# Kernel optimization log

Measured on AMD Instinct MI355X. Metric: run time of the kernel, lower is better.

Reference implementation:

```python
import jax, jax.numpy as jnp
import numpy as np

B, T, D_IN, H, D_OUT, L = 256, 512, 64, 512, 1, 2


def _lstm_layer(xs, W_ih, W_hh, b):
    """xs: [T, B, D]; W_ih: [4H, D]; W_hh: [4H, H]; b: [4H] (b_ih + b_hh).
    PyTorch gate order: i, f, g, o. Returns (ys [T,B,H], h_T [B,H])."""
    Bsz = xs.shape[1]
    Hh = W_hh.shape[1]
    h0 = jnp.zeros((Bsz, Hh), xs.dtype)
    c0 = jnp.zeros((Bsz, Hh), xs.dtype)

    def step(carry, x_t):
        h, c = carry
        gates = x_t @ W_ih.T + h @ W_hh.T + b  # [B, 4H]
        i, f, g, o = jnp.split(gates, 4, axis=-1)
        i = jax.nn.sigmoid(i)
        f = jax.nn.sigmoid(f)
        g = jnp.tanh(g)
        o = jax.nn.sigmoid(o)
        c = f * c + i * g
        h = o * jnp.tanh(c)
        return (h, c), h

    (hT, _), ys = jax.lax.scan(step, (h0, c0), xs)
    return ys, hT


def setup_inputs() -> dict:
    key = jax.random.key(0)
    ks = jax.random.split(key, 12)
    s = 0.05  # small init to avoid gate saturation
    return {
        "x": jax.random.normal(ks[0], (B, T, D_IN), jnp.float32),
        "W_ih0": jax.random.normal(ks[1], (4 * H, D_IN), jnp.float32) * s,
        "W_hh0": jax.random.normal(ks[2], (4 * H, H), jnp.float32) * s,
        "b0": jax.random.normal(ks[3], (4 * H,), jnp.float32) * s,
        "W_ih1": jax.random.normal(ks[4], (4 * H, H), jnp.float32) * s,
        "W_hh1": jax.random.normal(ks[5], (4 * H, H), jnp.float32) * s,
        "b1": jax.random.normal(ks[6], (4 * H,), jnp.float32) * s,
        "fc1_w": jax.random.normal(ks[7], (H, H), jnp.float32) * s,
        "fc1_b": jax.random.normal(ks[8], (H,), jnp.float32) * s,
        "fc_w": jax.random.normal(ks[9], (D_OUT, H), jnp.float32) * s,
        "fc_b": jax.random.normal(ks[10], (D_OUT,), jnp.float32) * s,
    }


def reference(x, W_ih0, W_hh0, b0, W_ih1, W_hh1, b1, fc1_w, fc1_b, fc_w, fc_b):
    xs = jnp.swapaxes(x, 0, 1)  # [T, B, D_IN]
    ys0, _ = _lstm_layer(xs, W_ih0, W_hh0, b0)      # [T, B, H]
    _, hT = _lstm_layer(ys0, W_ih1, W_hh1, b1)      # [B, H] == out[:, -1, :]
    h = jax.nn.relu(hT @ fc1_w.T + fc1_b)
    out = jax.nn.relu(h @ fc_w.T + fc_b)
    return out
```

## Files before the change

kernel.cpp:

```cpp
#include <hip/hip_runtime.h>
#include <stdint.h>


typedef __bf16 bf16;
typedef bf16  bf16x8 __attribute__((ext_vector_type(8)));
typedef float f32x4  __attribute__((ext_vector_type(4)));
typedef unsigned int u32;
typedef unsigned long long u64;

#define NB   256
#define NT   512
#define NDIN 64
#define NH   512
#define POLL_GUARD (1 << 20)
#define SLOT_BYTES ((size_t)NB * NH * 2)

static constexpr size_t OFF_XB   = 0;
static constexpr size_t OFF_WB0  = OFF_XB  + (size_t)NB*NT*NDIN*2;
static constexpr size_t OFF_WI0  = OFF_WB0 + (size_t)2048*512*2;
static constexpr size_t OFF_WI1  = OFF_WI0 + (size_t)2048*64*2;
static constexpr size_t OFF_WHS1 = OFF_WI1 + (size_t)2048*512*2;
static constexpr size_t OFF_Y0R  = OFF_WHS1+ (size_t)16*128*512*2;
static constexpr size_t OFF_R1   = OFF_Y0R + 2*SLOT_BYTES;
static constexpr size_t OFF_HT   = OFF_R1  + 2*SLOT_BYTES;
static constexpr size_t OFF_FLG  = OFF_HT  + (size_t)NB*NH*4;
static constexpr size_t WS_NEED  = OFF_FLG + 4096;

#define MFMA16(a,b,c) __builtin_amdgcn_mfma_f32_16x16x32_bf16(a,b,c,0,0,0)

__device__ __forceinline__ float fsigm(float x) {
    return __builtin_amdgcn_rcpf(1.0f + __builtin_amdgcn_exp2f(x * -1.442695041f));
}
__device__ __forceinline__ float ftanh(float x) {
    return 1.0f - 2.0f * __builtin_amdgcn_rcpf(1.0f + __builtin_amdgcn_exp2f(x * 2.885390082f));
}
__device__ __forceinline__ u32 pack_bf16(float a, float b) {
    union { bf16 h[2]; u32 u; } un;
    un.h[0] = (bf16)a; un.h[1] = (bf16)b;
    return un.u;
}
__device__ __forceinline__ bf16x8 asf(int4 x) {
    union { int4 i; bf16x8 v; } u; u.i = x; return u.v;
}

__device__ __forceinline__ void ld4_issue(const void* p0, const void* p1,
                                          const void* p2, const void* p3,
                                          int4& a, int4& b, int4& c, int4& d) {
    asm volatile(
        "global_load_dwordx4 %0, %4, off sc0 sc1\n\t"
        "global_load_dwordx4 %1, %5, off sc0 sc1\n\t"
        "global_load_dwordx4 %2, %6, off sc0 sc1\n\t"
        "global_load_dwordx4 %3, %7, off sc0 sc1"
        : "=&v"(a), "=&v"(b), "=&v"(c), "=&v"(d)
        : "v"(p0), "v"(p1), "v"(p2), "v"(p3)
        : "memory");
}
__device__ __forceinline__ void st64_cohr(void* p, u64 v) {
    asm volatile("global_store_dwordx2 %0, %1, off sc0 sc1" :: "v"(p), "v"(v) : "memory");
}
__device__ __forceinline__ void vm_drain() {
    asm volatile("s_waitcnt vmcnt(0)" ::: "memory");
    __builtin_amdgcn_sched_barrier(0);
}
__device__ __forceinline__ void ld_fence() {
    asm volatile("" ::: "memory");
    __builtin_amdgcn_sched_barrier(0);
}
__device__ __forceinline__ void poll64(const u32* f, u32 target) {
    int guard = 0;
    while (__hip_atomic_load(f, __ATOMIC_RELAXED, __HIP_MEMORY_SCOPE_AGENT) < target)
        if (++guard > POLL_GUARD) break;
}
__device__ __forceinline__ void ast32(u32* p, u32 v) {
    __hip_atomic_store(p, v, __ATOMIC_RELAXED, __HIP_MEMORY_SCOPE_AGENT);
}

__device__ __forceinline__ int wslot(int lr) {
    return ((lr >> 5) & 3) | (((lr >> 1) & 3) << 2);
}

__global__ void xcvt_kernel(const float* __restrict__ x, char* __restrict__ ws) {
    size_t i = ((size_t)blockIdx.x * 256 + threadIdx.x) * 8;
    float4 a = *(const float4*)(x + i);
    float4 b = *(const float4*)(x + i + 4);
    u32 p0 = pack_bf16(a.x, a.y), p1 = pack_bf16(a.z, a.w);
    u32 p2 = pack_bf16(b.x, b.y), p3 = pack_bf16(b.z, b.w);
    *(int4*)(ws + OFF_XB + i * 2) = make_int4((int)p0, (int)p1, (int)p2, (int)p3);
}

__global__ void prep_kernel(const float* __restrict__ Wih0f, const float* __restrict__ Whh0f,
                            const float* __restrict__ Wih1f, const float* __restrict__ Whh1f,
                            char* __restrict__ ws) {
    int idx = blockIdx.x * 256 + threadIdx.x;
    ((bf16*)(ws + OFF_WB0))[idx] = (bf16)Whh0f[idx];
    ((bf16*)(ws + OFF_WI1))[idx] = (bf16)Wih1f[idx];
    if (idx < 2048 * 64) ((bf16*)(ws + OFF_WI0))[idx] = (bf16)Wih0f[idx];
    int slice = idx >> 16;
    int lr    = (idx >> 9) & 127;
    int k     = idx & 511;
    int grow  = (lr >> 5) * 512 + slice * 32 + (lr & 31);
    ((bf16*)(ws + OFF_WHS1))[(size_t)slice * 65536 + lr * 512 + (k ^ (wslot(lr) << 3))] =
        (bf16)Whh1f[(size_t)grow * 512 + k];
}

__global__ __attribute__((amdgpu_waves_per_eu(1, 1))) __launch_bounds__(256)
void lstm_fused(const float* __restrict__ b0, const float* __restrict__ b1,
                char* __restrict__ ws) {
    extern __shared__ char smem[];
    char* WhLds = smem;
    char* hbufY = smem + 131072;
    char* hbufH = smem + 147456;

    const int tid = threadIdx.x;
    const int v = tid >> 6, l = tid & 63;
    const int l15 = l & 15, lhi = l >> 4, g = l & 3, csel = l15 >> 2;
    const int group = blockIdx.x >> 4, htile = blockIdx.x & 15;
    const int b0r = group * 16, hs = htile * 32;

    const bf16* xb = (const bf16*)(ws + OFF_XB);
    char* y0r = ws + OFF_Y0R;
    char* r1  = ws + OFF_R1;
    float* hT = (float*)(ws + OFF_HT);
    u32* FL = (u32*)(ws + OFF_FLG);
    const u32* myLine = FL + (size_t)group * 64;
    u32* peerF        = FL + (size_t)group * 64 + htile * 4 + v;

    {
        const char* wsrc = ws + OFF_WHS1 + (size_t)htile * 131072;
#pragma unroll
        for (int i = 0; i < 32; ++i) {
            int off = (tid + i * 256) * 16;
            *(int4*)(WhLds + off) = *(const int4*)(wsrc + off);
        }
    }

    const int wrow0 = g * 512 + hs + 8 * v + 2 * csel;
    const int wrow1 = wrow0 + 1;

    const bf16* wb0p = (const bf16*)(ws + OFF_WB0);
    const bf16* wi0p = (const bf16*)(ws + OFF_WI0);
    const bf16* wi1p = (const bf16*)(ws + OFF_WI1);
    int4 wb0[16][2], wib1[16][2];
#pragma unroll
    for (int kk = 0; kk < 16; ++kk) {
        wb0[kk][0]  = *(const int4*)(wb0p + (size_t)wrow0 * NH + kk * 32 + lhi * 8);
        wb0[kk][1]  = *(const int4*)(wb0p + (size_t)wrow1 * NH + kk * 32 + lhi * 8);
        wib1[kk][0] = *(const int4*)(wi1p + (size_t)wrow0 * NH + kk * 32 + lhi * 8);
        wib1[kk][1] = *(const int4*)(wi1p + (size_t)wrow1 * NH + kk * 32 + lhi * 8);
    }
    int4 wib0[2][2];
#pragma unroll
    for (int kk = 0; kk < 2; ++kk) {
        wib0[kk][0] = *(const int4*)(wi0p + (size_t)wrow0 * NDIN + kk * 32 + lhi * 8);
        wib0[kk][1] = *(const int4*)(wi0p + (size_t)wrow1 * NDIN + kk * 32 + lhi * 8);
    }
    const float b00 = b0[wrow0], b01 = b0[wrow1];
    const float b10 = b1[wrow0], b11 = b1[wrow1];

    float cA0[4] = {0,0,0,0}, cA1[4] = {0,0,0,0};
    float cB0[4] = {0,0,0,0}, cB1[4] = {0,0,0,0};
    f32x4 aL00, aL01, aL10, aL11;
    const int qb = l & 60;
    const int srcl = csel * 16 + g;
    const int swz = (l15 & 7) << 4;
    const int lr0 = g * 32 + 8 * v + 2 * csel;
    const int wsw = wslot(lr0) << 4;
    const int r0 = tid >> 6;
    const int bc = (tid & 63) * 16;

    int4 G0, G1, G2, G3;
    int4 H0, H1, H2, H3;

    auto issueG = [&](int slot) {
        const char* p = y0r + (size_t)slot * SLOT_BYTES + (size_t)b0r * 1024
                      + (size_t)r0 * 1024 + bc;
        ld4_issue(p, p + 4096, p + 8192, p + 12288, G0, G1, G2, G3);
    };
    auto issueH = [&](int slot) {
        const char* p = r1 + (size_t)slot * SLOT_BYTES + (size_t)b0r * 1024
                      + (size_t)r0 * 1024 + bc;
        ld4_issue(p, p + 4096, p + 8192, p + 12288, H0, H1, H2, H3);
    };
    auto ldsWrite = [&](char* buf, int4 A, int4 B, int4 C, int4 D) {
        *(int4*)(buf + (r0     ) * 1024 + (bc ^ (( r0      & 7) << 4))) = A;
        *(int4*)(buf + (r0 +  4) * 1024 + (bc ^ (((r0 + 4) & 7) << 4))) = B;
        *(int4*)(buf + (r0 +  8) * 1024 + (bc ^ (( r0      & 7) << 4))) = C;
        *(int4*)(buf + (r0 + 12) * 1024 + (bc ^ (((r0 + 4) & 7) << 4))) = D;
    };
    auto xproj0 = [&](int t) {
        const bf16* xp = xb + ((size_t)(b0r + l15) * NT + t) * NDIN + lhi * 8;
        bf16x8 xa0 = *(const bf16x8*)xp;
        bf16x8 xa1 = *(const bf16x8*)(xp + 32);
        aL00 = f32x4{b00, b00, b00, b00};
        aL01 = f32x4{b01, b01, b01, b01};
        aL00 = MFMA16(xa0, asf(wib0[0][0]), aL00); aL00 = MFMA16(xa1, asf(wib0[1][0]), aL00);
        aL01 = MFMA16(xa0, asf(wib0[0][1]), aL01); aL01 = MFMA16(xa1, asf(wib0[1][1]), aL01);
    };
    auto combine = [&](const f32x4& a0, const f32x4& a1, float* cc0, float* cc1,
                       float& h0s, float& h1s) {
        h0s = 0.f; h1s = 0.f;
#pragma unroll
        for (int j = 0; j < 4; ++j) {
            float va = a0[j];
            float gi = __shfl(va, qb), gf = __shfl(va, qb + 1);
            float gc = __shfl(va, qb + 2), go = __shfl(va, qb + 3);
            float cn = fsigm(gf) * cc0[j] + fsigm(gi) * ftanh(gc);
            cc0[j] = cn;
            float h = fsigm(go) * ftanh(cn);
            if (j == g) h0s = h;
            float vb = a1[j];
            gi = __shfl(vb, qb); gf = __shfl(vb, qb + 1);
            gc = __shfl(vb, qb + 2); go = __shfl(vb, qb + 3);
            cn = fsigm(gf) * cc1[j] + fsigm(gi) * ftanh(gc);
            cc1[j] = cn;
            h = fsigm(go) * ftanh(cn);
            if (j == g) h1s = h;
        }
    };
    auto publish = [&](float h0s, float h1s, char* tileBase) {
        u32 pk = pack_bf16(h0s, h1s);
        u32 w0 = __shfl(pk, srcl),     w1 = __shfl(pk, srcl + 4);
        u32 w2 = __shfl(pk, srcl + 8), w3 = __shfl(pk, srcl + 12);
        if (l < 16) {
            char* rp = tileBase + (size_t)l * 1024 + hs * 2 + v * 16;
            union { u32 w[2]; u64 q; } qa, qb2;
            qa.w[0] = w0; qa.w[1] = w1; qb2.w[0] = w2; qb2.w[1] = w3;
            st64_cohr(rp, qa.q); st64_cohr(rp + 8, qb2.q);
        }
    };
    auto setF = [&](u32 val) {
        if (l == 0) ast32(peerF, val);
    };

    __syncthreads();

    xproj0(0);
    {
        float h0s, h1s;
        combine(aL00, aL01, cA0, cA1, h0s, h1s);
        publish(h0s, h1s, y0r + (size_t)b0r * 1024);
        vm_drain();
        setF(1u);
        xproj0(1);
    }

    for (int e = 1; e <= NT; ++e) {
        const bool doL0 = (e < NT);
        const bool doH1 = (e >= 2);

        poll64(myLine + l, (u32)e);
        ld_fence();
        issueG((e - 1) & 1);
        if (doH1) issueH(e & 1);
        vm_drain();

        __syncthreads();
        ldsWrite(hbufY, G0, G1, G2, G3);
        if (doH1) ldsWrite(hbufH, H0, H1, H2, H3);
        __syncthreads();

        aL10 = f32x4{b10, b10, b10, b10};
        aL11 = f32x4{b11, b11, b11, b11};
#pragma unroll
        for (int kk = 0; kk < 16; ++kk) {
            bf16x8 ha = *(const bf16x8*)(hbufY + l15 * 1024 + ((kk * 64 + lhi * 16) ^ swz));
            if (doL0) {
                aL00 = MFMA16(ha, asf(wb0[kk][0]), aL00);
                aL01 = MFMA16(ha, asf(wb0[kk][1]), aL01);
            }
            aL10 = MFMA16(ha, asf(wib1[kk][0]), aL10);
            aL11 = MFMA16(ha, asf(wib1[kk][1]), aL11);
        }

        if (doL0) {
            float h0s, h1s;
            combine(aL00, aL01, cA0, cA1, h0s, h1s);
            publish(h0s, h1s, y0r + (size_t)(e & 1) * SLOT_BYTES + (size_t)b0r * 1024);
        }

        if (doH1) {
#pragma unroll
            for (int kk = 0; kk < 16; ++kk) {
                int kb = kk * 64 + lhi * 16;
                bf16x8 a  = *(const bf16x8*)(hbufH + l15 * 1024 + (kb ^ swz));
                bf16x8 w0 = *(const bf16x8*)(WhLds + (size_t) lr0      * 1024 + (kb ^ wsw));
                bf16x8 w1 = *(const bf16x8*)(WhLds + (size_t)(lr0 + 1) * 1024 + (kb ^ wsw));
                aL10 = MFMA16(a, w0, aL10);
                aL11 = MFMA16(a, w1, aL11);
            }
        }

        {
            float h0s, h1s;
            combine(aL10, aL11, cB0, cB1, h0s, h1s);
            if (e < NT) {
                publish(h0s, h1s, r1 + (size_t)((e - 1) & 1) * SLOT_BYTES + (size_t)b0r * 1024);
            } else {
                float* hp = hT + (size_t)(b0r + lhi * 4 + g) * NH + hs + 8 * v + 2 * csel;
                hp[0] = h0s; hp[1] = h1s;
            }
        }
        if (e < NT) {
            vm_drain();
            setF((u32)(e + 1));
            xproj0(e + 1);
        }
    }
}

__global__ __launch_bounds__(256) void fc_kernel(const float* __restrict__ fc1_w,
                                                 const float* __restrict__ fc1_b,
                                                 const float* __restrict__ fc_w,
                                                 const float* __restrict__ fc_b,
                                                 const char* __restrict__ ws,
                                                 float* __restrict__ out) {
    __shared__ float hLds[512];
    __shared__ float red[256];
    const int b = blockIdx.x, tid = threadIdx.x;
    const float* hT = (const float*)(ws + OFF_HT) + (size_t)b * NH;
    hLds[tid]       = hT[tid];
    hLds[tid + 256] = hT[tid + 256];
    __syncthreads();
    float p = 0.f;
#pragma unroll
    for (int rep = 0; rep < 2; ++rep) {
        int hh = tid + rep * 256;
        const float* wr = fc1_w + (size_t)hh * 512;
        float s = fc1_b[hh];
        for (int k = 0; k < 512; k += 4) {
            float4 w4 = *(const float4*)(wr + k);
            s += hLds[k] * w4.x + hLds[k + 1] * w4.y + hLds[k + 2] * w4.z + hLds[k + 3] * w4.w;
        }
        s = fmaxf(s, 0.f);
        p += s * fc_w[hh];
    }
    red[tid] = p;
    __syncthreads();
    for (int off = 128; off > 0; off >>= 1) {
        if (tid < off) red[tid] += red[tid + off];
        __syncthreads();
    }
    if (tid == 0) out[b] = fmaxf(red[0] + fc_b[0], 0.f);
}

extern "C" void kernel_launch(void* const* d_in, const int* in_sizes, int n_in,
                              void* d_out, int out_size, void* d_ws, size_t ws_size,
                              hipStream_t stream) {
    const float* x    = (const float*)d_in[0];
    const float* Wih0 = (const float*)d_in[1];
    const float* Whh0 = (const float*)d_in[2];
    const float* b0   = (const float*)d_in[3];
    const float* Wih1 = (const float*)d_in[4];
    const float* Whh1 = (const float*)d_in[5];
    const float* b1   = (const float*)d_in[6];
    const float* fc1w = (const float*)d_in[7];
    const float* fc1b = (const float*)d_in[8];
    const float* fcw  = (const float*)d_in[9];
    const float* fcb  = (const float*)d_in[10];
    char* ws = (char*)d_ws;
    float* out = (float*)d_out;

    if (ws_size < WS_NEED) {
        (void)hipMemsetAsync(d_out, 0, (size_t)out_size * 4, stream);
        return;
    }

    (void)hipMemsetAsync(ws + OFF_FLG, 0, 4096, stream);

    hipLaunchKernelGGL(xcvt_kernel, dim3(4096), dim3(256), 0, stream, x, ws);
    hipLaunchKernelGGL(prep_kernel, dim3(4096), dim3(256), 0, stream,
                       Wih0, Whh0, Wih1, Whh1, ws);
    hipLaunchKernelGGL(lstm_fused, dim3(256), dim3(256), 163840, stream, b0, b1, ws);
    hipLaunchKernelGGL(fc_kernel, dim3(256), dim3(256), 0, stream,
                       fc1w, fc1b, fcw, fcb, ws, out);
}
```

Baseline: 3.071 ms.

## Split layer-0 and layer-1 LSTM work into separate warp groups with LDS flags

Doubles the block to 512 threads so four waves run layer 0 and four waves run layer 1 concurrently, each with its own global flag lines. Block-wide __syncthreads is replaced by LDS counter handshakes, and the layer-1 recurrent h buffer is staged in two halves to fit shared memory. The goal is to overlap the two layers' recurrences and cut per-step register pressure by giving each wave half the weights. The cost is two waves per SIMD, more complex spin-wait synchronisation, and some risk of ordering bugs.

```diff
diff --git a/kernel.cpp b/kernel.cpp
--- a/kernel.cpp
+++ b/kernel.cpp
@@ -24,7 +24,7 @@
 static constexpr size_t OFF_R1   = OFF_Y0R + 2*SLOT_BYTES;
 static constexpr size_t OFF_HT   = OFF_R1  + 2*SLOT_BYTES;
 static constexpr size_t OFF_FLG  = OFF_HT  + (size_t)NB*NH*4;
-static constexpr size_t WS_NEED  = OFF_FLG + 4096;
+static constexpr size_t WS_NEED  = OFF_FLG + 8192;
 
 #define MFMA16(a,b,c) __builtin_amdgcn_mfma_f32_16x16x32_bf16(a,b,c,0,0,0)
 
@@ -73,6 +73,14 @@
 }
 __device__ __forceinline__ void ast32(u32* p, u32 v) {
     __hip_atomic_store(p, v, __ATOMIC_RELAXED, __HIP_MEMORY_SCOPE_AGENT);
+}
+__device__ __forceinline__ void lds_pollge(const u32* p, u32 target) {
+    int guard = 0;
+    while (__hip_atomic_load(p, __ATOMIC_ACQUIRE, __HIP_MEMORY_SCOPE_WORKGROUP) < target)
+        if (++guard > POLL_GUARD) break;
+}
+__device__ __forceinline__ void lds_add1(u32* p) {
+    __hip_atomic_fetch_add(p, 1u, __ATOMIC_RELEASE, __HIP_MEMORY_SCOPE_WORKGROUP);
 }
 
 __device__ __forceinline__ int wslot(int lr) {
@@ -103,99 +111,55 @@
         (bf16)Whh1f[(size_t)grow * 512 + k];
 }
 
-__global__ __attribute__((amdgpu_waves_per_eu(1, 1))) __launch_bounds__(256)
+__global__ __attribute__((amdgpu_waves_per_eu(2, 2))) __launch_bounds__(512)
 void lstm_fused(const float* __restrict__ b0, const float* __restrict__ b1,
                 char* __restrict__ ws) {
     extern __shared__ char smem[];
     char* WhLds = smem;
-    char* hbufY = smem + 131072;
-    char* hbufH = smem + 147456;
+    char* ybuf  = smem + 131072;
+    char* hbuf8 = smem + 147456;
+    u32* ydone = (u32*)(smem + 155648);
+    u32* yrd   = ydone + 16;
+    u32* hdone = ydone + 32;
+    u32* hrd   = ydone + 48;
 
     const int tid = threadIdx.x;
-    const int v = tid >> 6, l = tid & 63;
+    const int l = tid & 63;
+    const int v = (tid >> 6) & 3;
+    const bool isL0 = tid < 256;
     const int l15 = l & 15, lhi = l >> 4, g = l & 3, csel = l15 >> 2;
     const int group = blockIdx.x >> 4, htile = blockIdx.x & 15;
     const int b0r = group * 16, hs = htile * 32;
+    const int qb = l & 60;
+    const int srcl = csel * 16 + g;
+    const int swz = (l15 & 7) << 4;
+    const int r0 = v;
+    const int bc = l * 16;
 
     const bf16* xb = (const bf16*)(ws + OFF_XB);
     char* y0r = ws + OFF_Y0R;
     char* r1  = ws + OFF_R1;
     float* hT = (float*)(ws + OFF_HT);
     u32* FL = (u32*)(ws + OFF_FLG);
-    const u32* myLine = FL + (size_t)group * 64;
-    u32* peerF        = FL + (size_t)group * 64 + htile * 4 + v;
-
+    const u32* lineY = FL + (size_t)group * 64;
+    const u32* lineH = FL + 1024 + (size_t)group * 64;
+    u32* peerFY = FL + (size_t)group * 64 + htile * 4 + v;
+    u32* peerFH = FL + 1024 + (size_t)group * 64 + htile * 4 + v;
+
+    if (tid == 0) { ydone[0] = 0; yrd[0] = 0; hdone[0] = 0; hrd[0] = 0; }
     {
         const char* wsrc = ws + OFF_WHS1 + (size_t)htile * 131072;
 #pragma unroll
-        for (int i = 0; i < 32; ++i) {
-            int off = (tid + i * 256) * 16;
+        for (int i = 0; i < 16; ++i) {
+            int off = (tid + i * 512) * 16;
             *(int4*)(WhLds + off) = *(const int4*)(wsrc + off);
         }
     }
+    __syncthreads();
 
     const int wrow0 = g * 512 + hs + 8 * v + 2 * csel;
     const int wrow1 = wrow0 + 1;
 
-    const bf16* wb0p = (const bf16*)(ws + OFF_WB0);
-    const bf16* wi0p = (const bf16*)(ws + OFF_WI0);
-    const bf16* wi1p = (const bf16*)(ws + OFF_WI1);
-    int4 wb0[16][2], wib1[16][2];
-#pragma unroll
-    for (int kk = 0; kk < 16; ++kk) {
-        wb0[kk][0]  = *(const int4*)(wb0p + (size_t)wrow0 * NH + kk * 32 + lhi * 8);
-        wb0[kk][1]  = *(const int4*)(wb0p + (size_t)wrow1 * NH + kk * 32 + lhi * 8);
-        wib1[kk][0] = *(const int4*)(wi1p + (size_t)wrow0 * NH + kk * 32 + lhi * 8);
-        wib1[kk][1] = *(const int4*)(wi1p + (size_t)wrow1 * NH + kk * 32 + lhi * 8);
-    }
-    int4 wib0[2][2];
-#pragma unroll
-    for (int kk = 0; kk < 2; ++kk) {
-        wib0[kk][0] = *(const int4*)(wi0p + (size_t)wrow0 * NDIN + kk * 32 + lhi * 8);
-        wib0[kk][1] = *(const int4*)(wi0p + (size_t)wrow1 * NDIN + kk * 32 + lhi * 8);
-    }
-    const float b00 = b0[wrow0], b01 = b0[wrow1];
-    const float b10 = b1[wrow0], b11 = b1[wrow1];
-
-    float cA0[4] = {0,0,0,0}, cA1[4] = {0,0,0,0};
-    float cB0[4] = {0,0,0,0}, cB1[4] = {0,0,0,0};
-    f32x4 aL00, aL01, aL10, aL11;
-    const int qb = l & 60;
-    const int srcl = csel * 16 + g;
-    const int swz = (l15 & 7) << 4;
-    const int lr0 = g * 32 + 8 * v + 2 * csel;
-    const int wsw = wslot(lr0) << 4;
-    const int r0 = tid >> 6;
-    const int bc = (tid & 63) * 16;
-
-    int4 G0, G1, G2, G3;
-    int4 H0, H1, H2, H3;
-
-    auto issueG = [&](int slot) {
-        const char* p = y0r + (size_t)slot * SLOT_BYTES + (size_t)b0r * 1024
-                      + (size_t)r0 * 1024 + bc;
-        ld4_issue(p, p + 4096, p + 8192, p + 12288, G0, G1, G2, G3);
-    };
-    auto issueH = [&](int slot) {
-        const char* p = r1 + (size_t)slot * SLOT_BYTES + (size_t)b0r * 1024
-                      + (size_t)r0 * 1024 + bc;
-        ld4_issue(p, p + 4096, p + 8192, p + 12288, H0, H1, H2, H3);
-    };
-    auto ldsWrite = [&](char* buf, int4 A, int4 B, int4 C, int4 D) {
-        *(int4*)(buf + (r0     ) * 1024 + (bc ^ (( r0      & 7) << 4))) = A;
-        *(int4*)(buf + (r0 +  4) * 1024 + (bc ^ (((r0 + 4) & 7) << 4))) = B;
-        *(int4*)(buf + (r0 +  8) * 1024 + (bc ^ (( r0      & 7) << 4))) = C;
-        *(int4*)(buf + (r0 + 12) * 1024 + (bc ^ (((r0 + 4) & 7) << 4))) = D;
-    };
-    auto xproj0 = [&](int t) {
-        const bf16* xp = xb + ((size_t)(b0r + l15) * NT + t) * NDIN + lhi * 8;
-        bf16x8 xa0 = *(const bf16x8*)xp;
-        bf16x8 xa1 = *(const bf16x8*)(xp + 32);
-        aL00 = f32x4{b00, b00, b00, b00};
-        aL01 = f32x4{b01, b01, b01, b01};
-        aL00 = MFMA16(xa0, asf(wib0[0][0]), aL00); aL00 = MFMA16(xa1, asf(wib0[1][0]), aL00);
-        aL01 = MFMA16(xa0, asf(wib0[0][1]), aL01); aL01 = MFMA16(xa1, asf(wib0[1][1]), aL01);
-    };
     auto combine = [&](const f32x4& a0, const f32x4& a1, float* cc0, float* cc1,
                        float& h0s, float& h1s) {
         h0s = 0.f; h1s = 0.f;
@@ -228,82 +192,170 @@
             st64_cohr(rp, qa.q); st64_cohr(rp + 8, qb2.q);
         }
     };
-    auto setF = [&](u32 val) {
-        if (l == 0) ast32(peerF, val);
-    };
-
-    __syncthreads();
-
-    xproj0(0);
-    {
-        float h0s, h1s;
-        combine(aL00, aL01, cA0, cA1, h0s, h1s);
-        publish(h0s, h1s, y0r + (size_t)b0r * 1024);
-        vm_drain();
-        setF(1u);
-        xproj0(1);
-    }
-
-    for (int e = 1; e <= NT; ++e) {
-        const bool doL0 = (e < NT);
-        const bool doH1 = (e >= 2);
-
-        poll64(myLine + l, (u32)e);
-        ld_fence();
-        issueG((e - 1) & 1);
-        if (doH1) issueH(e & 1);
-        vm_drain();
-
-        __syncthreads();
-        ldsWrite(hbufY, G0, G1, G2, G3);
-        if (doH1) ldsWrite(hbufH, H0, H1, H2, H3);
-        __syncthreads();
-
-        aL10 = f32x4{b10, b10, b10, b10};
-        aL11 = f32x4{b11, b11, b11, b11};
+
+    if (isL0) {
+        const bf16* wb0p = (const bf16*)(ws + OFF_WB0);
+        const bf16* wi0p = (const bf16*)(ws + OFF_WI0);
+        int4 wb0[16][2];
 #pragma unroll
         for (int kk = 0; kk < 16; ++kk) {
-            bf16x8 ha = *(const bf16x8*)(hbufY + l15 * 1024 + ((kk * 64 + lhi * 16) ^ swz));
-            if (doL0) {
-                aL00 = MFMA16(ha, asf(wb0[kk][0]), aL00);
-                aL01 = MFMA16(ha, asf(wb0[kk][1]), aL01);
-            }
-            aL10 = MFMA16(ha, asf(wib1[kk][0]), aL10);
-            aL11 = MFMA16(ha, asf(wib1[kk][1]), aL11);
-        }
-
-        if (doL0) {
+            wb0[kk][0] = *(const int4*)(wb0p + (size_t)wrow0 * NH + kk * 32 + lhi * 8);
+            wb0[kk][1] = *(const int4*)(wb0p + (size_t)wrow1 * NH + kk * 32 + lhi * 8);
+        }
+        int4 wib0[2][2];
+#pragma unroll
+        for (int kk = 0; kk < 2; ++kk) {
+            wib0[kk][0] = *(const int4*)(wi0p + (size_t)wrow0 * NDIN + kk * 32 + lhi * 8);
+            wib0[kk][1] = *(const int4*)(wi0p + (size_t)wrow1 * NDIN + kk * 32 + lhi * 8);
+        }
+        const float b00 = b0[wrow0], b01 = b0[wrow1];
+        float cA0[4] = {0,0,0,0}, cA1[4] = {0,0,0,0};
+        f32x4 aL00, aL01;
+        int4 G0, G1, G2, G3;
+
+        auto xproj0 = [&](int t) {
+            const bf16* xp = xb + ((size_t)(b0r + l15) * NT + t) * NDIN + lhi * 8;
+            bf16x8 xa0 = *(const bf16x8*)xp;
+            bf16x8 xa1 = *(const bf16x8*)(xp + 32);
+            aL00 = f32x4{b00, b00, b00, b00};
+            aL01 = f32x4{b01, b01, b01, b01};
+            aL00 = MFMA16(xa0, asf(wib0[0][0]), aL00); aL00 = MFMA16(xa1, asf(wib0[1][0]), aL00);
+            aL01 = MFMA16(xa0, asf(wib0[0][1]), aL01); aL01 = MFMA16(xa1, asf(wib0[1][1]), aL01);
+        };
+        auto issueG = [&](int slot) {
+            const char* p = y0r + (size_t)slot * SLOT_BYTES + (size_t)b0r * 1024
+                          + (size_t)r0 * 1024 + bc;
+            ld4_issue(p, p + 4096, p + 8192, p + 12288, G0, G1, G2, G3);
+        };
+
+        xproj0(0);
+        {
             float h0s, h1s;
             combine(aL00, aL01, cA0, cA1, h0s, h1s);
-            publish(h0s, h1s, y0r + (size_t)(e & 1) * SLOT_BYTES + (size_t)b0r * 1024);
-        }
-
-        if (doH1) {
+            publish(h0s, h1s, y0r + (size_t)b0r * 1024);
+            vm_drain();
+            if (l == 0) ast32(peerFY, 1u);
+            xproj0(1);
+        }
+
+        for (int e = 1; e <= NT; ++e) {
+            poll64(lineY + l, (u32)e);
+            ld_fence();
+            issueG((e - 1) & 1);
+            lds_pollge(yrd, 8u * (e - 1));
+            vm_drain();
+            *(int4*)(ybuf + (r0     ) * 1024 + (bc ^ (( r0      & 7) << 4))) = G0;
+            *(int4*)(ybuf + (r0 +  4) * 1024 + (bc ^ (((r0 + 4) & 7) << 4))) = G1;
+            *(int4*)(ybuf + (r0 +  8) * 1024 + (bc ^ (( r0      & 7) << 4))) = G2;
+            *(int4*)(ybuf + (r0 + 12) * 1024 + (bc ^ (((r0 + 4) & 7) << 4))) = G3;
+            if (l == 0) lds_add1(ydone);
+            lds_pollge(ydone, 4u * e);
+
+            if (e < NT) {
+                aL00 = aL00; aL01 = aL01;
+#pragma unroll
+                for (int kk = 0; kk < 16; ++kk) {
+                    bf16x8 ha = *(const bf16x8*)(ybuf + l15 * 1024 + ((kk * 64 + lhi * 16) ^ swz));
+                    aL00 = MFMA16(ha, asf(wb0[kk][0]), aL00);
+                    aL01 = MFMA16(ha, asf(wb0[kk][1]), aL01);
+                }
+                if (l == 0) lds_add1(yrd);
+                float h0s, h1s;
+                combine(aL00, aL01, cA0, cA1, h0s, h1s);
+                publish(h0s, h1s, y0r + (size_t)(e & 1) * SLOT_BYTES + (size_t)b0r * 1024);
+                vm_drain();
+                if (l == 0) ast32(peerFY, (u32)(e + 1));
+                if (e + 1 < NT) xproj0(e + 1);
+            }
+        }
+    } else {
+        const bf16* wi1p = (const bf16*)(ws + OFF_WI1);
+        int4 wib1[16][2];
+#pragma unroll
+        for (int kk = 0; kk < 16; ++kk) {
+            wib1[kk][0] = *(const int4*)(wi1p + (size_t)wrow0 * NH + kk * 32 + lhi * 8);
+            wib1[kk][1] = *(const int4*)(wi1p + (size_t)wrow1 * NH + kk * 32 + lhi * 8);
+        }
+        const float b10 = b1[wrow0], b11 = b1[wrow1];
+        const int lr0 = g * 32 + 8 * v + 2 * csel;
+        const int wsw = wslot(lr0) << 4;
+        float cB0[4] = {0,0,0,0}, cB1[4] = {0,0,0,0};
+        f32x4 aL10, aL11;
+        int4 H0, H1, H2, H3;
+        const int rA = v + 4 * (l >> 5);
+        const int ch = (l & 31) * 16;
+
+        auto issueHx = [&](int slot) {
+            const char* base = r1 + (size_t)slot * SLOT_BYTES + (size_t)b0r * 1024;
+            const char* p0 = base + (size_t)rA * 1024 + ch;
+            const char* p1 = base + (size_t)(rA + 8) * 1024 + ch;
+            ld4_issue(p0, p1, p0 + 512, p1 + 512, H0, H1, H2, H3);
+        };
+        auto writeHalf = [&](int4 X, int4 Y) {
+            *(int4*)(hbuf8 + (size_t)rA * 512 + (ch ^ ((rA & 7) << 4))) = X;
+            *(int4*)(hbuf8 + (size_t)(rA + 8) * 512 + (ch ^ (((rA + 8) & 7) << 4))) = Y;
+        };
+
+        for (int e = 1; e <= NT; ++e) {
+            if (e >= 2) {
+                poll64(lineH + l, (u32)(e - 1));
+                ld_fence();
+                issueHx(e & 1);
+            }
+            aL10 = f32x4{b10, b10, b10, b10};
+            aL11 = f32x4{b11, b11, b11, b11};
+            lds_pollge(ydone, 4u * e);
 #pragma unroll
             for (int kk = 0; kk < 16; ++kk) {
-                int kb = kk * 64 + lhi * 16;
-                bf16x8 a  = *(const bf16x8*)(hbufH + l15 * 1024 + (kb ^ swz));
-                bf16x8 w0 = *(const bf16x8*)(WhLds + (size_t) lr0      * 1024 + (kb ^ wsw));
-                bf16x8 w1 = *(const bf16x8*)(WhLds + (size_t)(lr0 + 1) * 1024 + (kb ^ wsw));
-                aL10 = MFMA16(a, w0, aL10);
-                aL11 = MFMA16(a, w1, aL11);
+                bf16x8 ha = *(const bf16x8*)(ybuf + l15 * 1024 + ((kk * 64 + lhi * 16) ^ swz));
+                aL10 = MFMA16(ha, asf(wib1[kk][0]), aL10);
+                aL11 = MFMA16(ha, asf(wib1[kk][1]), aL11);
             }
-        }
-
-        {
+            if (l == 0) lds_add1(yrd);
+
+            if (e >= 2) {
+                u32 U = (u32)(e - 2);
+                vm_drain();
+                lds_pollge(hrd, 8u * U);
+                writeHalf(H0, H1);
+                if (l == 0) lds_add1(hdone);
+                lds_pollge(hdone, 8u * U + 4);
+#pragma unroll
+                for (int kk = 0; kk < 8; ++kk) {
+                    int kb = kk * 64 + lhi * 16;
+                    bf16x8 a  = *(const bf16x8*)(hbuf8 + l15 * 512 + (kb ^ swz));
+                    bf16x8 w0 = *(const bf16x8*)(WhLds + (size_t) lr0      * 1024 + (kb ^ wsw));
+                    bf16x8 w1 = *(const bf16x8*)(WhLds + (size_t)(lr0 + 1) * 1024 + (kb ^ wsw));
+                    aL10 = MFMA16(a, w0, aL10);
+                    aL11 = MFMA16(a, w1, aL11);
+                }
+                if (l == 0) lds_add1(hrd);
+                lds_pollge(hrd, 8u * U + 4);
+                writeHalf(H2, H3);
+                if (l == 0) lds_add1(hdone);
+                lds_pollge(hdone, 8u * U + 8);
+#pragma unroll
+                for (int kk = 8; kk < 16; ++kk) {
+                    int kb = kk * 64 + lhi * 16;
+                    bf16x8 a  = *(const bf16x8*)(hbuf8 + l15 * 512 + (((kk - 8) * 64 + lhi * 16) ^ swz));
+                    bf16x8 w0 = *(const bf16x8*)(WhLds + (size_t) lr0      * 1024 + (kb ^ wsw));
+                    bf16x8 w1 = *(const bf16x8*)(WhLds + (size_t)(lr0 + 1) * 1024 + (kb ^ wsw));
+                    aL10 = MFMA16(a, w0, aL10);
+                    aL11 = MFMA16(a, w1, aL11);
+                }
+                if (l == 0) lds_add1(hrd);
+            }
+
             float h0s, h1s;
             combine(aL10, aL11, cB0, cB1, h0s, h1s);
             if (e < NT) {
                 publish(h0s, h1s, r1 + (size_t)((e - 1) & 1) * SLOT_BYTES + (size_t)b0r * 1024);
+                vm_drain();
+                if (l == 0) ast32(peerFH, (u32)e);
             } else {
                 float* hp = hT + (size_t)(b0r + lhi * 4 + g) * NH + hs + 8 * v + 2 * csel;
                 hp[0] = h0s; hp[1] = h1s;
             }
-        }
-        if (e < NT) {
-            vm_drain();
-            setF((u32)(e + 1));
-            xproj0(e + 1);
         }
     }
 }
@@ -365,12 +417,12 @@
         return;
     }
 
-    (void)hipMemsetAsync(ws + OFF_FLG, 0, 4096, stream);
+    (void)hipMemsetAsync(ws + OFF_FLG, 0, 8192, stream);
 
     hipLaunchKernelGGL(xcvt_kernel, dim3(4096), dim3(256), 0, stream, x, ws);
     hipLaunchKernelGGL(prep_kernel, dim3(4096), dim3(256), 0, stream,
                        Wih0, Whh0, Wih1, Whh1, ws);
-    hipLaunchKernelGGL(lstm_fused, dim3(256), dim3(256), 163840, stream, b0, b1, ws);
+    hipLaunchKernelGGL(lstm_fused, dim3(256), dim3(512), 155712, stream, b0, b1, ws);
     hipLaunchKernelGGL(fc_kernel, dim3(256), dim3(256), 0, stream,
                        fc1w, fc1b, fcw, fcb, ws, out);
 }
```

New measurement: 3.653 ms. 18.9% more time.

## Split layer-0 and layer-1 readiness flags to publish layer-0 output earlier

Applied to the files above, without the earlier changes.

Replaces the single per-step flag with two separate flag lines, one for layer-0 outputs and one for layer-1 outputs. Layer 0's matmul and combine now run first, and its flag is raised before layer-1 work, so peers can start fetching the next layer-0 state sooner. Polling and global loads for the next step move to the end of the current step. The intent is to shorten the critical path in the cross-block wavefront pipeline. It costs extra flag traffic, an extra drain per step and more complicated ordering.

```diff
diff --git a/kernel.cpp b/kernel.cpp
--- a/kernel.cpp
+++ b/kernel.cpp
@@ -24,7 +24,7 @@
 static constexpr size_t OFF_R1   = OFF_Y0R + 2*SLOT_BYTES;
 static constexpr size_t OFF_HT   = OFF_R1  + 2*SLOT_BYTES;
 static constexpr size_t OFF_FLG  = OFF_HT  + (size_t)NB*NH*4;
-static constexpr size_t WS_NEED  = OFF_FLG + 4096;
+static constexpr size_t WS_NEED  = OFF_FLG + 8192;
 
 #define MFMA16(a,b,c) __builtin_amdgcn_mfma_f32_16x16x32_bf16(a,b,c,0,0,0)
 
@@ -122,8 +122,10 @@
     char* r1  = ws + OFF_R1;
     float* hT = (float*)(ws + OFF_HT);
     u32* FL = (u32*)(ws + OFF_FLG);
-    const u32* myLine = FL + (size_t)group * 64;
-    u32* peerF        = FL + (size_t)group * 64 + htile * 4 + v;
+    const u32* lineY = FL + (size_t)group * 64;
+    const u32* lineH = FL + 1024 + (size_t)group * 64;
+    u32* peerFY = FL + (size_t)group * 64 + htile * 4 + v;
+    u32* peerFH = FL + 1024 + (size_t)group * 64 + htile * 4 + v;
 
     {
         const char* wsrc = ws + OFF_WHS1 + (size_t)htile * 131072;
@@ -228,9 +230,6 @@
             st64_cohr(rp, qa.q); st64_cohr(rp + 8, qb2.q);
         }
     };
-    auto setF = [&](u32 val) {
-        if (l == 0) ast32(peerF, val);
-    };
 
     __syncthreads();
 
@@ -240,44 +239,43 @@
         combine(aL00, aL01, cA0, cA1, h0s, h1s);
         publish(h0s, h1s, y0r + (size_t)b0r * 1024);
         vm_drain();
-        setF(1u);
+        if (l == 0) ast32(peerFY, 1u);
         xproj0(1);
+        poll64(lineY + l, 1u);
+        ld_fence();
+        issueG(0);
     }
 
     for (int e = 1; e <= NT; ++e) {
         const bool doL0 = (e < NT);
         const bool doH1 = (e >= 2);
 
-        poll64(myLine + l, (u32)e);
-        ld_fence();
-        issueG((e - 1) & 1);
-        if (doH1) issueH(e & 1);
         vm_drain();
-
         __syncthreads();
         ldsWrite(hbufY, G0, G1, G2, G3);
         if (doH1) ldsWrite(hbufH, H0, H1, H2, H3);
         __syncthreads();
 
-        aL10 = f32x4{b10, b10, b10, b10};
-        aL11 = f32x4{b11, b11, b11, b11};
-#pragma unroll
-        for (int kk = 0; kk < 16; ++kk) {
-            bf16x8 ha = *(const bf16x8*)(hbufY + l15 * 1024 + ((kk * 64 + lhi * 16) ^ swz));
-            if (doL0) {
+        if (doL0) {
+#pragma unroll
+            for (int kk = 0; kk < 16; ++kk) {
+                bf16x8 ha = *(const bf16x8*)(hbufY + l15 * 1024 + ((kk * 64 + lhi * 16) ^ swz));
                 aL00 = MFMA16(ha, asf(wb0[kk][0]), aL00);
                 aL01 = MFMA16(ha, asf(wb0[kk][1]), aL01);
             }
-            aL10 = MFMA16(ha, asf(wib1[kk][0]), aL10);
-            aL11 = MFMA16(ha, asf(wib1[kk][1]), aL11);
-        }
-
-        if (doL0) {
             float h0s, h1s;
             combine(aL00, aL01, cA0, cA1, h0s, h1s);
             publish(h0s, h1s, y0r + (size_t)(e & 1) * SLOT_BYTES + (size_t)b0r * 1024);
         }
 
+        aL10 = f32x4{b10, b10, b10, b10};
+        aL11 = f32x4{b11, b11, b11, b11};
+#pragma unroll
+        for (int kk = 0; kk < 16; ++kk) {
+            bf16x8 ha = *(const bf16x8*)(hbufY + l15 * 1024 + ((kk * 64 + lhi * 16) ^ swz));
+            aL10 = MFMA16(ha, asf(wib1[kk][0]), aL10);
+            aL11 = MFMA16(ha, asf(wib1[kk][1]), aL11);
+        }
         if (doH1) {
 #pragma unroll
             for (int kk = 0; kk < 16; ++kk) {
@@ -290,20 +288,27 @@
             }
         }
 
+        vm_drain();
+        if (doL0 && l == 0) ast32(peerFY, (u32)(e + 1));
+
         {
             float h0s, h1s;
             combine(aL10, aL11, cB0, cB1, h0s, h1s);
             if (e < NT) {
                 publish(h0s, h1s, r1 + (size_t)((e - 1) & 1) * SLOT_BYTES + (size_t)b0r * 1024);
+                vm_drain();
+                if (l == 0) ast32(peerFH, (u32)e);
+                poll64(lineY + l, (u32)(e + 1));
+                ld_fence();
+                issueG(e & 1);
+                poll64(lineH + l, (u32)e);
+                ld_fence();
+                issueH((e + 1) & 1);
+                if (e + 1 < NT) xproj0(e + 1);
             } else {
                 float* hp = hT + (size_t)(b0r + lhi * 4 + g) * NH + hs + 8 * v + 2 * csel;
                 hp[0] = h0s; hp[1] = h1s;
             }
-        }
-        if (e < NT) {
-            vm_drain();
-            setF((u32)(e + 1));
-            xproj0(e + 1);
         }
     }
 }
@@ -365,7 +370,7 @@
         return;
     }
 
-    (void)hipMemsetAsync(ws + OFF_FLG, 0, 4096, stream);
+    (void)hipMemsetAsync(ws + OFF_FLG, 0, 8192, stream);
 
     hipLaunchKernelGGL(xcvt_kernel, dim3(4096), dim3(256), 0, stream, x, ws);
     hipLaunchKernelGGL(prep_kernel, dim3(4096), dim3(256), 0, stream,
```

Measured after the change: 3.557 ms. 1.16x slower.
